# Optimization experiments

Measured on AMD Instinct MI355X. Metric: run time of the kernel, lower is better.

## Reference

```python
import jax, jax.numpy as jnp
import numpy as np

B, T, E, H = 4, 2048, 1024, 16
S = E // H  # 64


def setup_inputs() -> dict:
    key = jax.random.key(0)
    ks = jax.random.split(key, 6)
    return {
        "x": jax.random.normal(ks[0], (B, T, E), dtype=jnp.float32),
        "Wk": jax.random.normal(ks[1], (S, S), dtype=jnp.float32) * (1.0 / np.sqrt(S)),
        "Wq": jax.random.normal(ks[2], (S, S), dtype=jnp.float32) * (1.0 / np.sqrt(S)),
        "Wv": jax.random.normal(ks[3], (S, S), dtype=jnp.float32) * (1.0 / np.sqrt(S)),
        "Wp": jax.random.normal(ks[4], (E, E), dtype=jnp.float32) * (1.0 / np.sqrt(E)),
        "bp": jnp.zeros((E,), dtype=jnp.float32),
    }


def reference(x, Wk, Wq, Wv, Wp, bp):
    b, t, e = x.shape
    h, s = H, S
    xh = x.reshape(b, t, h, s)
    # per-head projections share one (s,s) weight across all heads (torch Linear: y = x @ W.T)
    keys = jnp.einsum('bthi,oi->bhto', xh, Wk)     # (b,h,t,s)
    queries = jnp.einsum('bthi,oi->bhto', xh, Wq)
    values = jnp.einsum('bthi,oi->bhto', xh, Wv)
    scale = e ** 0.25  # q and k each divided by e^(1/4) -> net 1/sqrt(e)
    queries = queries / scale
    keys = keys / scale
    dot = jnp.einsum('bhqs,bhks->bhqk', queries, keys)  # (b,h,t,t)
    attn = jax.nn.softmax(dot, axis=-1)
    out = jnp.einsum('bhqk,bhks->bqhs', attn, values)   # (b,t,h,s)
    out = out.reshape(b, t, h * s)
    return jnp.einsum('bte,oe->bto', out, Wp) + bp
```

## Files before the change

### kernel.cpp

```cpp
#include <hip/hip_runtime.h>
#include <hip/hip_bf16.h>

#define Bv 4
#define Tv 2048
#define Ev 1024
#define Hv 16
#define Sv 64

typedef __attribute__((ext_vector_type(8))) short bf16x8;
typedef __attribute__((ext_vector_type(4))) short bf16x4;
typedef __attribute__((ext_vector_type(4))) float f32x4;
typedef __attribute__((ext_vector_type(16))) float f32x16;

__device__ __forceinline__ ushort f2bf(float f) {
    unsigned u = __float_as_uint(f);
    u = (u + 0x7FFFu + ((u >> 16) & 1u)) >> 16;
    return (ushort)u;
}
__device__ __forceinline__ unsigned pkrn(float a, float b) {
    __hip_bfloat162 t = __float22bfloat162_rn(make_float2(a, b));
    unsigned r; __builtin_memcpy(&r, &t, 4); return r;
}
__device__ __forceinline__ unsigned pktr(float a, float b) {
    return __builtin_amdgcn_perm(__float_as_uint(b), __float_as_uint(a), 0x07060302u);
}

__device__ __forceinline__ void async16(void* lds, const void* g) {
    __builtin_amdgcn_global_load_lds(
        (const __attribute__((address_space(1))) unsigned int*)g,
        (__attribute__((address_space(3))) unsigned int*)lds, 16, 0, 0);
}

__global__ __launch_bounds__(256) void cast_kernel(
    const float* __restrict__ Wp, const float* __restrict__ Wq,
    const float* __restrict__ Wk, const float* __restrict__ Wv,
    ushort* __restrict__ Wpb, ushort* __restrict__ Wqb,
    ushort* __restrict__ Wkb, ushort* __restrict__ Wvb)
{
    int blk = blockIdx.x;
    if (blk < 1024) {
        int i = (blk * 256 + threadIdx.x) * 4;
        float4 v = *(const float4*)(Wp + i);
        uint2 o = {pkrn(v.x, v.y), pkrn(v.z, v.w)};
        *(uint2*)(Wpb + i) = o;
    } else {
        int p = blk - 1024;
        const float* src = (p == 0) ? Wq : ((p == 1) ? Wk : Wv);
        ushort* dst      = (p == 0) ? Wqb : ((p == 1) ? Wkb : Wvb);
        const float scale = (p == 0) ? 0.03125f * 1.4426950408889634f : 1.0f;
        #pragma unroll
        for (int it = 0; it < 4; ++it) {
            int i = (it * 256 + threadIdx.x) * 4;
            float4 v = *(const float4*)(src + i);
            uint2 o = {pkrn(v.x * scale, v.y * scale), pkrn(v.z * scale, v.w * scale)};
            *(uint2*)(dst + i) = o;
        }
    }
}

__global__ __launch_bounds__(192) void qkv_kernel(
    const float* __restrict__ x,
    const ushort* __restrict__ Wqb, const ushort* __restrict__ Wkb,
    const ushort* __restrict__ Wvb,
    ushort* __restrict__ Q, ushort* __restrict__ K, ushort* __restrict__ Vt)
{
    const int tid  = threadIdx.x;
    const int wave = tid >> 6;
    const int lane = tid & 63;
    const int m    = lane & 15;
    const int quad = lane >> 4;

    const ushort* Wsel = (wave == 0) ? Wqb : ((wave == 1) ? Wkb : Wvb);
    bf16x8 wf[4][2];
    #pragma unroll
    for (int ot = 0; ot < 4; ++ot)
        #pragma unroll
        for (int ks = 0; ks < 2; ++ks)
            wf[ot][ks] = *(const bf16x8*)&Wsel[(ot * 16 + m) * 64 + ks * 32 + quad * 8];

    const int tt = blockIdx.x >> 2;
    const int hg = blockIdx.x & 3;
    const int g0 = tt * 16;
    const int gm = g0 + m;
    const int b  = g0 >> 11;
    const int t0 = g0 & 2047;

    #pragma unroll
    for (int hi = 0; hi < 4; ++hi) {
        const int h  = hg * 4 + hi;
        const int bh = b * Hv + h;

        bf16x8 xf[2];
        #pragma unroll
        for (int ks = 0; ks < 2; ++ks) {
            const float* src = x + (size_t)gm * Ev + h * Sv + ks * 32 + quad * 8;
            float4 v0 = *(const float4*)src;
            float4 v1 = *(const float4*)(src + 4);
            unsigned pk[4];
            pk[0] = pkrn(v0.x, v0.y); pk[1] = pkrn(v0.z, v0.w);
            pk[2] = pkrn(v1.x, v1.y); pk[3] = pkrn(v1.z, v1.w);
            xf[ks] = *(bf16x8*)pk;
        }

        f32x4 acc[4];
        #pragma unroll
        for (int ot = 0; ot < 4; ++ot) acc[ot] = (f32x4){0.f, 0.f, 0.f, 0.f};

        if (wave < 2) {
            #pragma unroll
            for (int ks = 0; ks < 2; ++ks)
                #pragma unroll
                for (int ot = 0; ot < 4; ++ot)
                    acc[ot] = __builtin_amdgcn_mfma_f32_16x16x32_bf16(
                        wf[ot][ks], xf[ks], acc[ot], 0, 0, 0);
            ushort* dst = ((wave == 0) ? Q : K)
                        + ((size_t)bh * Tv + t0 + m) * Sv + quad * 4;
            #pragma unroll
            for (int ot = 0; ot < 4; ++ot) {
                uint2 w = {pkrn(acc[ot][0], acc[ot][1]), pkrn(acc[ot][2], acc[ot][3])};
                *(uint2*)(dst + ot * 16) = w;
            }
        } else {
            #pragma unroll
            for (int ks = 0; ks < 2; ++ks)
                #pragma unroll
                for (int st = 0; st < 4; ++st)
                    acc[st] = __builtin_amdgcn_mfma_f32_16x16x32_bf16(
                        xf[ks], wf[st][ks], acc[st], 0, 0, 0);
            ushort* vr = Vt + ((size_t)bh * Sv + m) * Tv + t0 + quad * 4;
            #pragma unroll
            for (int st = 0; st < 4; ++st) {
                uint2 w = {pkrn(acc[st][0], acc[st][1]), pkrn(acc[st][2], acc[st][3])};
                *(uint2*)(vr + (size_t)st * 16 * Tv) = w;
            }
        }
    }
}

__global__ __launch_bounds__(256, 2) void attn_kernel(
    const ushort* __restrict__ Q, const ushort* __restrict__ K,
    const ushort* __restrict__ Vt, ushort* __restrict__ O)
{
    __shared__ ushort kl[2][64 * 64];
    __shared__ ushort vl[2][64 * 64];
    __shared__ float  ll[4][64];

    const int tid  = threadIdx.x;
    const int wave = tid >> 6;
    const int lane = tid & 63;
    const int r31  = lane & 31;
    const int hi   = lane >> 5;
    const int bh   = blockIdx.x & 63;
    const int q0   = (blockIdx.x >> 6) << 8;

    const ushort* Qb = Q + ((size_t)bh * Tv + q0 + wave * 64 + r31) * Sv + hi * 8;
    bf16x8 qf[2][4];
    #pragma unroll
    for (int g = 0; g < 2; ++g)
        #pragma unroll
        for (int ks = 0; ks < 4; ++ks)
            qf[g][ks] = *(const bf16x8*)(Qb + (size_t)g * 32 * Sv + ks * 16);

    f32x16 oa[2][2];
    #pragma unroll
    for (int g = 0; g < 2; ++g)
        #pragma unroll
        for (int st = 0; st < 2; ++st)
            #pragma unroll
            for (int r = 0; r < 16; ++r)
                oa[g][st][r] = 0.f;
    float lsum[2] = {0.f, 0.f};

    const ushort* Kb = K  + (size_t)bh * Tv * Sv;
    const ushort* Vb = Vt + (size_t)bh * Sv * Tv;

    const int r0 = tid >> 3,         cg0 = (tid & 7) ^ (r0 & 7);
    const int r1 = (256 + tid) >> 3, cg1 = ((256 + tid) & 7) ^ (r1 & 7);
    const size_t koff0 = (size_t)r0 * Sv + cg0 * 8;
    const size_t koff1 = (size_t)r1 * Sv + cg1 * 8;
    const size_t voff0 = (size_t)r0 * Tv + cg0 * 8;
    const size_t voff1 = (size_t)r1 * Tv + cg1 * 8;
    const int swz = r31 & 7;

    auto softpv = [&](const f32x16& sv, float& ls, f32x16* oag, int kp,
                      const bf16x8* vf) {
        float p[8];
        #pragma unroll
        for (int j = 0; j < 8; ++j)
            p[j] = __builtin_amdgcn_exp2f(sv[kp * 8 + j]);
        ls += ((p[0] + p[1]) + (p[2] + p[3]))
            + ((p[4] + p[5]) + (p[6] + p[7]));
        unsigned d0 = pktr(p[0], p[1]);
        unsigned d1 = pktr(p[2], p[3]);
        unsigned d2 = pktr(p[4], p[5]);
        unsigned d3 = pktr(p[6], p[7]);
        asm volatile("v_permlane32_swap_b32 %0, %1" : "+v"(d0), "+v"(d2));
        asm volatile("v_permlane32_swap_b32 %0, %1" : "+v"(d1), "+v"(d3));
        unsigned pw[4] = {d0, d1, d2, d3};
        bf16x8 pf = *(bf16x8*)pw;
        #pragma unroll
        for (int st = 0; st < 2; ++st)
            oag[st] = __builtin_amdgcn_mfma_f32_32x32x16_bf16(
                pf, vf[st], oag[st], 0, 0, 0);
    };

    uint4 rk0 = *(const uint4*)(Kb + koff0);
    uint4 rk1 = *(const uint4*)(Kb + koff1);
    uint4 rv0 = *(const uint4*)(Vb + voff0);
    uint4 rv1 = *(const uint4*)(Vb + voff1);
    *(uint4*)&kl[0][(size_t)tid * 8]         = rk0;
    *(uint4*)&kl[0][((size_t)tid + 256) * 8] = rk1;
    *(uint4*)&vl[0][(size_t)tid * 8]         = rv0;
    *(uint4*)&vl[0][((size_t)tid + 256) * 8] = rv1;
    rk0 = *(const uint4*)(Kb + (size_t)64 * Sv + koff0);
    rk1 = *(const uint4*)(Kb + (size_t)64 * Sv + koff1);
    rv0 = *(const uint4*)(Vb + 64 + voff0);
    rv1 = *(const uint4*)(Vb + 64 + voff1);
    __syncthreads();

    for (int k0 = 0; k0 < Tv; k0 += 64) {
        const int cur = (k0 >> 6) & 1;

        *(uint4*)&kl[cur ^ 1][(size_t)tid * 8]         = rk0;
        *(uint4*)&kl[cur ^ 1][((size_t)tid + 256) * 8] = rk1;
        *(uint4*)&vl[cur ^ 1][(size_t)tid * 8]         = rv0;
        *(uint4*)&vl[cur ^ 1][((size_t)tid + 256) * 8] = rv1;

        int kn = k0 + 128; if (kn >= Tv) kn = 0;
        rk0 = *(const uint4*)(Kb + (size_t)kn * Sv + koff0);
        rk1 = *(const uint4*)(Kb + (size_t)kn * Sv + koff1);
        rv0 = *(const uint4*)(Vb + kn + voff0);
        rv1 = *(const uint4*)(Vb + kn + voff1);

        #pragma unroll
        for (int kt = 0; kt < 2; ++kt) {
            bf16x8 kf[4];
            #pragma unroll
            for (int ks = 0; ks < 4; ++ks)
                kf[ks] = *(const bf16x8*)
                    &kl[cur][(kt * 32 + r31) * 64 + (((ks * 2 + hi) ^ swz) * 8)];

            f32x16 s0, s1;
            #pragma unroll
            for (int r = 0; r < 16; ++r) { s0[r] = 0.f; s1[r] = 0.f; }
            #pragma unroll
            for (int ks = 0; ks < 4; ++ks)
                s0 = __builtin_amdgcn_mfma_f32_32x32x16_bf16(
                    kf[ks], qf[0][ks], s0, 0, 0, 0);
            #pragma unroll
            for (int ks = 0; ks < 4; ++ks)
                s1 = __builtin_amdgcn_mfma_f32_32x32x16_bf16(
                    kf[ks], qf[1][ks], s1, 0, 0, 0);

            #pragma unroll
            for (int kp = 0; kp < 2; ++kp) {
                const int kc = (kt * 2 + kp) * 2 + hi;
                bf16x8 vf[2];
                #pragma unroll
                for (int st = 0; st < 2; ++st)
                    vf[st] = *(const bf16x8*)
                        &vl[cur][(st * 32 + r31) * 64 + ((kc ^ swz) * 8)];
                softpv(s0, lsum[0], oa[0], kp, vf);
                softpv(s1, lsum[1], oa[1], kp, vf);
            }
        }

        __syncthreads();
    }

    lsum[0] += __shfl_xor(lsum[0], 32, 64);
    lsum[1] += __shfl_xor(lsum[1], 32, 64);
    if (hi == 0) {
        ll[wave][r31]      = 1.0f / lsum[0];
        ll[wave][32 + r31] = 1.0f / lsum[1];
    }

    const int b = bh >> 4, h = bh & 15;
    #pragma unroll
    for (int g = 0; g < 2; ++g) {
        float sc[16];
        #pragma unroll
        for (int r = 0; r < 16; ++r)
            sc[r] = ll[wave][g * 32 + (r & 3) + 4 * hi + 8 * (r >> 2)];
        #pragma unroll
        for (int st = 0; st < 2; ++st)
            #pragma unroll
            for (int r = 0; r < 16; ++r) {
                const int q = (r & 3) + 4 * hi + 8 * (r >> 2);
                O[((size_t)(b * Tv + q0 + wave * 64 + g * 32 + q)) * Ev
                  + h * Sv + st * 32 + r31] = f2bf(oa[g][st][r] * sc[r]);
            }
    }
}

__global__ __launch_bounds__(256) void proj_kernel(
    const ushort* __restrict__ A, const ushort* __restrict__ B,
    const float* __restrict__ bp, float* __restrict__ C)
{
    __shared__ ushort Asm[128 * 32];
    __shared__ ushort Bsm[128 * 32];
    const int tid  = threadIdx.x;
    const int wave = tid >> 6;
    const int lane = tid & 63;
    const int m    = lane & 15;
    const int quad = lane >> 4;
    const int wm   = wave >> 1;
    const int wn   = wave & 1;
    const int m0   = blockIdx.x * 128;
    const int n0   = blockIdx.y * 128;

    f32x4 acc[4][4];
    #pragma unroll
    for (int i = 0; i < 4; ++i)
        #pragma unroll
        for (int j = 0; j < 4; ++j)
            acc[i][j] = (f32x4){0.f, 0.f, 0.f, 0.f};

    for (int k0 = 0; k0 < Ev; k0 += 32) {
        __syncthreads();
        #pragma unroll
        for (int j = 0; j < 2; ++j) {
            int c   = j * 256 + tid;
            int row = c >> 2;
            int col = (c & 3) * 8;
            async16(&Asm[c * 8], &A[(size_t)(m0 + row) * Ev + k0 + col]);
            async16(&Bsm[c * 8], &B[(size_t)(n0 + row) * Ev + k0 + col]);
        }
        __syncthreads();

        bf16x8 af[4], bf[4];
        #pragma unroll
        for (int i = 0; i < 4; ++i)
            af[i] = *(const bf16x8*)&Asm[(wm * 64 + i * 16 + m) * 32 + quad * 8];
        #pragma unroll
        for (int j = 0; j < 4; ++j)
            bf[j] = *(const bf16x8*)&Bsm[(wn * 64 + j * 16 + m) * 32 + quad * 8];
        #pragma unroll
        for (int i = 0; i < 4; ++i)
            #pragma unroll
            for (int j = 0; j < 4; ++j)
                acc[i][j] = __builtin_amdgcn_mfma_f32_16x16x32_bf16(
                    af[i], bf[j], acc[i][j], 0, 0, 0);
    }

    float bbv[4];
    #pragma unroll
    for (int j = 0; j < 4; ++j)
        bbv[j] = bp[n0 + wn * 64 + j * 16 + m];

    #pragma unroll
    for (int i = 0; i < 4; ++i)
        #pragma unroll
        for (int j = 0; j < 4; ++j)
            #pragma unroll
            for (int r = 0; r < 4; ++r)
                C[(size_t)(m0 + wm * 64 + i * 16 + quad * 4 + r) * Ev
                  + n0 + wn * 64 + j * 16 + m] = acc[i][j][r] + bbv[j];
}

extern "C" void kernel_launch(void* const* d_in, const int* in_sizes, int n_in,
                              void* d_out, int out_size, void* d_ws, size_t ws_size,
                              hipStream_t stream) {
    const float* x  = (const float*)d_in[0];
    const float* Wk = (const float*)d_in[1];
    const float* Wq = (const float*)d_in[2];
    const float* Wv = (const float*)d_in[3];
    const float* Wp = (const float*)d_in[4];
    const float* bp = (const float*)d_in[5];
    float* out = (float*)d_out;

    ushort* Q   = (ushort*)d_ws;
    ushort* K   = Q   + 8388608;
    ushort* Vt  = K   + 8388608;
    ushort* O   = Vt  + 8388608;
    ushort* Wpb = O   + 8388608;
    ushort* Wqb = Wpb + 1048576;
    ushort* Wkb = Wqb + 4096;
    ushort* Wvb = Wkb + 4096;

    cast_kernel<<<1027, 256, 0, stream>>>(Wp, Wq, Wk, Wv, Wpb, Wqb, Wkb, Wvb);
    qkv_kernel<<<2048, 192, 0, stream>>>(x, Wqb, Wkb, Wvb, Q, K, Vt);
    attn_kernel<<<512, 256, 0, stream>>>(Q, K, Vt, O);
    proj_kernel<<<dim3(64, 8), 256, 0, stream>>>(O, Wpb, bp, out);
}
```

Baseline: 220.4 us.

## Fuse weight casts into QKV kernel, stage x via LDS, double-buffer proj GEMM

The separate cast kernel is removed. The Wp bf16 cast now runs in extra blocks of the QKV launch, and the small Q/K/V weights are cast and scaled inside each QKV block. The QKV kernel stages its x tile through LDS with async loads and an XOR swizzle, and it changes the Q/K MFMA operand order, which turns the Q/K stores into scalar 16-bit writes. The projection GEMM switches from async LDS loads to a register-prefetched double-buffered LDS pipeline with one barrier per iteration. Together these aim to cut a launch and overlap global loads with MFMA work, at the cost of redundant per-block weight casting and narrower stores.

```diff
diff --git a/kernel.cpp b/kernel.cpp
--- a/kernel.cpp
+++ b/kernel.cpp
@@ -8,7 +8,6 @@
 #define Sv 64
 
 typedef __attribute__((ext_vector_type(8))) short bf16x8;
-typedef __attribute__((ext_vector_type(4))) short bf16x4;
 typedef __attribute__((ext_vector_type(4))) float f32x4;
 typedef __attribute__((ext_vector_type(16))) float f32x16;
 
@@ -31,59 +30,69 @@
         (__attribute__((address_space(3))) unsigned int*)lds, 16, 0, 0);
 }
 
-__global__ __launch_bounds__(256) void cast_kernel(
-    const float* __restrict__ Wp, const float* __restrict__ Wq,
-    const float* __restrict__ Wk, const float* __restrict__ Wv,
-    ushort* __restrict__ Wpb, ushort* __restrict__ Wqb,
-    ushort* __restrict__ Wkb, ushort* __restrict__ Wvb)
-{
-    int blk = blockIdx.x;
-    if (blk < 1024) {
-        int i = (blk * 256 + threadIdx.x) * 4;
-        float4 v = *(const float4*)(Wp + i);
-        uint2 o = {pkrn(v.x, v.y), pkrn(v.z, v.w)};
-        *(uint2*)(Wpb + i) = o;
-    } else {
-        int p = blk - 1024;
-        const float* src = (p == 0) ? Wq : ((p == 1) ? Wk : Wv);
-        ushort* dst      = (p == 0) ? Wqb : ((p == 1) ? Wkb : Wvb);
-        const float scale = (p == 0) ? 0.03125f * 1.4426950408889634f : 1.0f;
-        #pragma unroll
-        for (int it = 0; it < 4; ++it) {
-            int i = (it * 256 + threadIdx.x) * 4;
-            float4 v = *(const float4*)(src + i);
-            uint2 o = {pkrn(v.x * scale, v.y * scale), pkrn(v.z * scale, v.w * scale)};
-            *(uint2*)(dst + i) = o;
-        }
-    }
-}
-
 __global__ __launch_bounds__(192) void qkv_kernel(
     const float* __restrict__ x,
-    const ushort* __restrict__ Wqb, const ushort* __restrict__ Wkb,
-    const ushort* __restrict__ Wvb,
+    const float* __restrict__ Wq, const float* __restrict__ Wk,
+    const float* __restrict__ Wv, const float* __restrict__ Wp,
+    ushort* __restrict__ Wpb,
     ushort* __restrict__ Q, ushort* __restrict__ K, ushort* __restrict__ Vt)
 {
+    if (blockIdx.x >= 2048) {
+        size_t i = ((size_t)(blockIdx.x - 2048) * 192 + threadIdx.x) * 8;
+        if (i < (size_t)Ev * Ev) {
+            float4 v0 = *(const float4*)(Wp + i);
+            float4 v1 = *(const float4*)(Wp + i + 4);
+            uint4 o = {pkrn(v0.x, v0.y), pkrn(v0.z, v0.w),
+                       pkrn(v1.x, v1.y), pkrn(v1.z, v1.w)};
+            *(uint4*)(Wpb + i) = o;
+        }
+        return;
+    }
+
+    __shared__ float xs[16 * 256];
+
     const int tid  = threadIdx.x;
     const int wave = tid >> 6;
     const int lane = tid & 63;
     const int m    = lane & 15;
     const int quad = lane >> 4;
 
-    const ushort* Wsel = (wave == 0) ? Wqb : ((wave == 1) ? Wkb : Wvb);
-    bf16x8 wf[4][2];
-    #pragma unroll
-    for (int ot = 0; ot < 4; ++ot)
-        #pragma unroll
-        for (int ks = 0; ks < 2; ++ks)
-            wf[ot][ks] = *(const bf16x8*)&Wsel[(ot * 16 + m) * 64 + ks * 32 + quad * 8];
-
     const int tt = blockIdx.x >> 2;
     const int hg = blockIdx.x & 3;
     const int g0 = tt * 16;
-    const int gm = g0 + m;
     const int b  = g0 >> 11;
     const int t0 = g0 & 2047;
+
+    #pragma unroll
+    for (int pass = 0; pass < 6; ++pass) {
+        int c = pass * 192 + tid;
+        if (c < 1024) {
+            int tok  = c >> 6;
+            int gsrc = (c & 63) ^ (tok & 7);
+            async16(&xs[c * 4],
+                    x + (size_t)(g0 + tok) * Ev + hg * 256 + gsrc * 4);
+        }
+    }
+
+    const float* Wsel = (wave == 0) ? Wq : ((wave == 1) ? Wk : Wv);
+    const float wscale = (wave == 0) ? 0.03125f * 1.4426950408889634f : 1.0f;
+    bf16x8 wf[4][2];
+    #pragma unroll
+    for (int ot = 0; ot < 4; ++ot)
+        #pragma unroll
+        for (int ks = 0; ks < 2; ++ks) {
+            const float* ws = &Wsel[(ot * 16 + m) * 64 + ks * 32 + quad * 8];
+            float4 w0 = *(const float4*)ws;
+            float4 w1 = *(const float4*)(ws + 4);
+            unsigned pk[4];
+            pk[0] = pkrn(w0.x * wscale, w0.y * wscale);
+            pk[1] = pkrn(w0.z * wscale, w0.w * wscale);
+            pk[2] = pkrn(w1.x * wscale, w1.y * wscale);
+            pk[3] = pkrn(w1.z * wscale, w1.w * wscale);
+            wf[ot][ks] = *(bf16x8*)pk;
+        }
+
+    __syncthreads();
 
     #pragma unroll
     for (int hi = 0; hi < 4; ++hi) {
@@ -93,9 +102,9 @@
         bf16x8 xf[2];
         #pragma unroll
         for (int ks = 0; ks < 2; ++ks) {
-            const float* src = x + (size_t)gm * Ev + h * Sv + ks * 32 + quad * 8;
-            float4 v0 = *(const float4*)src;
-            float4 v1 = *(const float4*)(src + 4);
+            int gc = hi * 16 + ks * 8 + quad * 2;
+            float4 v0 = *(const float4*)&xs[(m * 64 + ( gc      ^ (m & 7))) * 4];
+            float4 v1 = *(const float4*)&xs[(m * 64 + ((gc + 1) ^ (m & 7))) * 4];
             unsigned pk[4];
             pk[0] = pkrn(v0.x, v0.y); pk[1] = pkrn(v0.z, v0.w);
             pk[2] = pkrn(v1.x, v1.y); pk[3] = pkrn(v1.z, v1.w);
@@ -112,14 +121,14 @@
                 #pragma unroll
                 for (int ot = 0; ot < 4; ++ot)
                     acc[ot] = __builtin_amdgcn_mfma_f32_16x16x32_bf16(
-                        wf[ot][ks], xf[ks], acc[ot], 0, 0, 0);
-            ushort* dst = ((wave == 0) ? Q : K)
-                        + ((size_t)bh * Tv + t0 + m) * Sv + quad * 4;
-            #pragma unroll
-            for (int ot = 0; ot < 4; ++ot) {
-                uint2 w = {pkrn(acc[ot][0], acc[ot][1]), pkrn(acc[ot][2], acc[ot][3])};
-                *(uint2*)(dst + ot * 16) = w;
-            }
+                        xf[ks], wf[ot][ks], acc[ot], 0, 0, 0);
+            ushort* dst = ((wave == 0) ? Q : K) + ((size_t)bh * Tv + t0) * Sv;
+            #pragma unroll
+            for (int ot = 0; ot < 4; ++ot)
+                #pragma unroll
+                for (int r = 0; r < 4; ++r)
+                    dst[(quad * 4 + r) * Sv + ot * 16 + m]
+                        = (ushort)pkrn(acc[ot][r], acc[ot][r]);
         } else {
             #pragma unroll
             for (int ks = 0; ks < 2; ++ks)
@@ -294,11 +303,11 @@
 }
 
 __global__ __launch_bounds__(256) void proj_kernel(
-    const ushort* __restrict__ A, const ushort* __restrict__ B,
+    const ushort* __restrict__ A, const ushort* __restrict__ Bw,
     const float* __restrict__ bp, float* __restrict__ C)
 {
-    __shared__ ushort Asm[128 * 32];
-    __shared__ ushort Bsm[128 * 32];
+    __shared__ ushort Asm[2][128 * 32];
+    __shared__ ushort Bsm[2][128 * 32];
     const int tid  = threadIdx.x;
     const int wave = tid >> 6;
     const int lane = tid & 63;
@@ -316,31 +325,52 @@
         for (int j = 0; j < 4; ++j)
             acc[i][j] = (f32x4){0.f, 0.f, 0.f, 0.f};
 
-    for (int k0 = 0; k0 < Ev; k0 += 32) {
-        __syncthreads();
-        #pragma unroll
-        for (int j = 0; j < 2; ++j) {
-            int c   = j * 256 + tid;
-            int row = c >> 2;
-            int col = (c & 3) * 8;
-            async16(&Asm[c * 8], &A[(size_t)(m0 + row) * Ev + k0 + col]);
-            async16(&Bsm[c * 8], &B[(size_t)(n0 + row) * Ev + k0 + col]);
-        }
-        __syncthreads();
+    const int row0 = tid >> 2,         col0 = (tid & 3) * 8;
+    const int row1 = (256 + tid) >> 2, col1 = ((256 + tid) & 3) * 8;
+
+    uint4 a0 = *(const uint4*)&A [(size_t)(m0 + row0) * Ev + col0];
+    uint4 a1 = *(const uint4*)&A [(size_t)(m0 + row1) * Ev + col1];
+    uint4 b0 = *(const uint4*)&Bw[(size_t)(n0 + row0) * Ev + col0];
+    uint4 b1 = *(const uint4*)&Bw[(size_t)(n0 + row1) * Ev + col1];
+    *(uint4*)&Asm[0][(size_t)tid * 8]         = a0;
+    *(uint4*)&Asm[0][((size_t)tid + 256) * 8] = a1;
+    *(uint4*)&Bsm[0][(size_t)tid * 8]         = b0;
+    *(uint4*)&Bsm[0][((size_t)tid + 256) * 8] = b1;
+    a0 = *(const uint4*)&A [(size_t)(m0 + row0) * Ev + 32 + col0];
+    a1 = *(const uint4*)&A [(size_t)(m0 + row1) * Ev + 32 + col1];
+    b0 = *(const uint4*)&Bw[(size_t)(n0 + row0) * Ev + 32 + col0];
+    b1 = *(const uint4*)&Bw[(size_t)(n0 + row1) * Ev + 32 + col1];
+    __syncthreads();
+
+    for (int it = 0; it < 32; ++it) {
+        const int cur = it & 1;
+        if (it < 31) {
+            *(uint4*)&Asm[cur ^ 1][(size_t)tid * 8]         = a0;
+            *(uint4*)&Asm[cur ^ 1][((size_t)tid + 256) * 8] = a1;
+            *(uint4*)&Bsm[cur ^ 1][(size_t)tid * 8]         = b0;
+            *(uint4*)&Bsm[cur ^ 1][((size_t)tid + 256) * 8] = b1;
+            int kn = (it + 2) * 32; if (kn >= Ev) kn = 0;
+            a0 = *(const uint4*)&A [(size_t)(m0 + row0) * Ev + kn + col0];
+            a1 = *(const uint4*)&A [(size_t)(m0 + row1) * Ev + kn + col1];
+            b0 = *(const uint4*)&Bw[(size_t)(n0 + row0) * Ev + kn + col0];
+            b1 = *(const uint4*)&Bw[(size_t)(n0 + row1) * Ev + kn + col1];
+        }
 
         bf16x8 af[4], bf[4];
         #pragma unroll
         for (int i = 0; i < 4; ++i)
-            af[i] = *(const bf16x8*)&Asm[(wm * 64 + i * 16 + m) * 32 + quad * 8];
+            af[i] = *(const bf16x8*)&Asm[cur][(wm * 64 + i * 16 + m) * 32 + quad * 8];
         #pragma unroll
         for (int j = 0; j < 4; ++j)
-            bf[j] = *(const bf16x8*)&Bsm[(wn * 64 + j * 16 + m) * 32 + quad * 8];
+            bf[j] = *(const bf16x8*)&Bsm[cur][(wn * 64 + j * 16 + m) * 32 + quad * 8];
         #pragma unroll
         for (int i = 0; i < 4; ++i)
             #pragma unroll
             for (int j = 0; j < 4; ++j)
                 acc[i][j] = __builtin_amdgcn_mfma_f32_16x16x32_bf16(
                     af[i], bf[j], acc[i][j], 0, 0, 0);
+
+        __syncthreads();
     }
 
     float bbv[4];
@@ -374,12 +404,8 @@
     ushort* Vt  = K   + 8388608;
     ushort* O   = Vt  + 8388608;
     ushort* Wpb = O   + 8388608;
-    ushort* Wqb = Wpb + 1048576;
-    ushort* Wkb = Wqb + 4096;
-    ushort* Wvb = Wkb + 4096;
-
-    cast_kernel<<<1027, 256, 0, stream>>>(Wp, Wq, Wk, Wv, Wpb, Wqb, Wkb, Wvb);
-    qkv_kernel<<<2048, 192, 0, stream>>>(x, Wqb, Wkb, Wvb, Q, K, Vt);
+
+    qkv_kernel<<<2731, 192, 0, stream>>>(x, Wq, Wk, Wv, Wp, Wpb, Q, K, Vt);
     attn_kernel<<<512, 256, 0, stream>>>(Q, K, Vt, O);
     proj_kernel<<<dim3(64, 8), 256, 0, stream>>>(O, Wpb, bp, out);
 }
```

Measured after the change: 205.8 us. 6.6% less time.
